# Kernel tuning notes

Hardware: AMD Instinct MI355X
Metric: run time of the kernel (lower is better)

The kernel has to match this reference:

```python
import jax, jax.numpy as jnp
import numpy as np

H, C, PQ, PV = 12, 16, 4, 8
CN = 384
INF, EPS = 1e5, 1e-7


def setup_inputs() -> dict:
    key = jax.random.key(0)
    ks = jax.random.split(key, 12)
    B, N = 2, 768
    s = jax.random.normal(ks[0], (B, N, CN), jnp.float32)
    m = jax.random.normal(ks[1], (B, N, 3, 3), jnp.float32)
    rot, _ = jnp.linalg.qr(m)  # proper orthonormal frames
    trans = jax.random.normal(ks[2], (B, N, 3), jnp.float32)
    pair_mask = jnp.ones((B, N, N), jnp.float32)
    sc = 0.02
    hc = H * C
    w_q = jax.random.normal(ks[3], (hc, CN), jnp.float32) * sc
    b_q = jnp.zeros((hc,), jnp.float32)
    w_kv = jax.random.normal(ks[4], (2 * hc, CN), jnp.float32) * sc
    b_kv = jnp.zeros((2 * hc,), jnp.float32)
    w_qp = jax.random.normal(ks[5], (H * PQ * 3, CN), jnp.float32) * sc
    b_qp = jnp.zeros((H * PQ * 3,), jnp.float32)
    w_kvp = jax.random.normal(ks[6], (H * (PQ + PV) * 3, CN), jnp.float32) * sc
    b_kvp = jnp.zeros((H * (PQ + PV) * 3,), jnp.float32)
    head_weights = jnp.full((H,), float(np.log(np.e - 1.0)), jnp.float32)  # softplus -> 1
    cod = H * (C + PV * 4)
    w_out = jax.random.normal(ks[7], (CN, cod), jnp.float32) * sc
    b_out = jnp.zeros((CN,), jnp.float32)
    return dict(s=s, rot=rot, trans=trans, pair_mask=pair_mask,
                w_q=w_q, b_q=b_q, w_kv=w_kv, b_kv=b_kv,
                w_qp=w_qp, b_qp=b_qp, w_kvp=w_kvp, b_kvp=b_kvp,
                head_weights=head_weights, w_out=w_out, b_out=b_out)


def reference(s, rot, trans, pair_mask, w_q, b_q, w_kv, b_kv, w_qp, b_qp,
              w_kvp, b_kvp, head_weights, w_out, b_out):
    B, N, _ = s.shape
    q = (s @ w_q.T + b_q).reshape(B, N, H, C)
    kv = (s @ w_kv.T + b_kv).reshape(B, N, H, 2 * C)
    k, v = kv[..., :C], kv[..., C:]

    def point_proj(wf, bf, P):
        p = s @ wf.T + bf                                   # [B,N,H*P*3]
        p = jnp.stack(jnp.split(p, 3, axis=-1), axis=-1)     # [B,N,H*P,3]
        p = jnp.einsum('bnxy,bnpy->bnpx', rot, p) + trans[:, :, None, :]
        return p.reshape(B, N, H, P, 3)

    q_pts = point_proj(w_qp, b_qp, PQ)
    kv_pts = point_proj(w_kvp, b_kvp, PQ + PV)
    k_pts, v_pts = kv_pts[..., :PQ, :], kv_pts[..., PQ:, :]

    a = jnp.einsum('bihc,bjhc->bhij', q, k) * (1.0 / (3 * C)) ** 0.5
    # [B,N,N,H,PQ] squared point distances (the big intermediate)
    d2 = jnp.sum((q_pts[:, :, None] - k_pts[:, None]) ** 2, axis=-1)
    hw = jax.nn.softplus(head_weights) * (1.0 / (3 * (PQ * 9.0 / 2))) ** 0.5
    pt_att = -0.5 * jnp.sum(d2 * hw[:, None], axis=-1)      # [B,N,N,H]
    a = a + jnp.transpose(pt_att, (0, 3, 1, 2)) + (INF * (pair_mask - 1.0))[:, None]
    a = jax.nn.softmax(a, axis=-1)                          # [B,H,N,N]

    o = jnp.einsum('bhij,bjhc->bihc', a, v).reshape(B, N, H * C)
    o_pt = jnp.einsum('bhij,bjhpc->bihpc', a, v_pts)        # [B,N,H,PV,3]
    o_pt = jnp.einsum('bnyx,bnhpy->bnhpx', rot, o_pt - trans[:, :, None, None, :])
    o_pt_norm = jnp.sqrt(jnp.sum(o_pt ** 2, axis=-1) + EPS).reshape(B, N, H * PV)
    o_pt = o_pt.reshape(B, N, H * PV, 3)
    cat = jnp.concatenate([o, o_pt[..., 0], o_pt[..., 1], o_pt[..., 2], o_pt_norm], axis=-1)
    return cat @ w_out.T + b_out
```

## Files before the change

kernel.cpp:

```cpp
#include <hip/hip_runtime.h>
#include <hip/hip_bf16.h>
#include <math.h>

typedef __attribute__((ext_vector_type(4)))  short short4v;
typedef __attribute__((ext_vector_type(8)))  short short8;
typedef __attribute__((ext_vector_type(16))) float f32x16;

#define B_   2
#define N_   768
#define CN_  384
#define H_   12
#define INF_ 100000.0f
#define EPS_ 1e-7f

#define OFF_PROJ 0
#define OFF_O    589824
#define OFF_OP   737280
#define OFF_CAT  958464
#define OFF_QF   1769472
#define OFF_KF   2064384
#define OFF_VT   2359296
#define OFF_SB   2949120
#define OFF_WB   3244032
#define OFF_WOB  3465216
#define OFF_MB   3575808

__device__ inline float b2f(unsigned short u) {
    union { unsigned int i; float f; } x; x.i = ((unsigned int)u) << 16; return x.f;
}
__device__ inline unsigned short f2b(float f) {
    __hip_bfloat16 h = __float2bfloat16(f);
    return *reinterpret_cast<unsigned short*>(&h);
}

__global__ __launch_bounds__(256) void prep_kernel(
    const float* __restrict__ s,
    const float* __restrict__ w_q,  const float* __restrict__ w_kv,
    const float* __restrict__ w_qp, const float* __restrict__ w_kvp,
    const float* __restrict__ w_out,
    unsigned short* __restrict__ SB, unsigned short* __restrict__ WB,
    unsigned short* __restrict__ WOBT)
{
    const long i4 = ((long)blockIdx.x * 256 + threadIdx.x) * 4;
    const float* src; unsigned short* dst; long off;
    if (i4 < 589824) {
        src = s + i4; dst = SB; off = i4;
    } else if (i4 < 1032192) {
        long e = i4 - 589824;
        int row = (int)(e / 384), c = (int)(e - (long)row * 384);
        const float* wsrc;
        if (row < 192)      wsrc = w_q   + (long)row * 384;
        else if (row < 576) wsrc = w_kv  + (long)(row - 192) * 384;
        else if (row < 720) wsrc = w_qp  + (long)(row - 576) * 384;
        else                wsrc = w_kvp + (long)(row - 720) * 384;
        src = wsrc + c; dst = WB; off = e;
    } else {
        long e = i4 - 1032192;
        int row = (int)(e / 576), c = (int)(e - (long)row * 576);
        src = w_out + e; dst = WOBT;
        off = (((long)(row >> 5) * 72 + (c >> 3)) * 32 + (row & 31)) * 8 + (c & 7);
    }
    float4 v = *(const float4*)src;
    short4v o;
    o[0] = (short)f2b(v.x); o[1] = (short)f2b(v.y);
    o[2] = (short)f2b(v.z); o[3] = (short)f2b(v.w);
    *(short4v*)(dst + off) = o;
}

__global__ __launch_bounds__(64) void proj_mb_kernel(
    const unsigned short* __restrict__ SB, const unsigned short* __restrict__ WB,
    const float* __restrict__ b_q,  const float* __restrict__ b_kv,
    const float* __restrict__ b_qp, const float* __restrict__ b_kvp,
    const float* __restrict__ mask,
    float* __restrict__ proj, unsigned short* __restrict__ MB)
{
    if (blockIdx.x >= 1728) {
        const int tile = blockIdx.x - 1728;
        const int jt = tile % 24;
        const int it = (tile / 24) % 24;
        const int b  = tile / 576;
        const int tt = threadIdx.x;
        const int i0 = it * 32, j0 = jt * 32;
        const float* mrow = mask + ((long)b * N_ + i0 + (tt & 31)) * N_
                          + j0 + (tt >> 5) * 4;
        union { unsigned short u[16]; short8 v[2]; } o;
        #pragma unroll
        for (int g = 0; g < 4; ++g) {
            float4 mv = *(const float4*)(mrow + 8 * g);
            o.u[g*4+0] = f2b(INF_ * (mv.x - 1.f));
            o.u[g*4+1] = f2b(INF_ * (mv.y - 1.f));
            o.u[g*4+2] = f2b(INF_ * (mv.z - 1.f));
            o.u[g*4+3] = f2b(INF_ * (mv.w - 1.f));
        }
        unsigned short* outp = MB + (long)tile * 1024 + tt * 16;
        *(short8*)(outp)     = o.v[0];
        *(short8*)(outp + 8) = o.v[1];
        return;
    }
    const int tile = blockIdx.x;
    const int tn = tile % 36, tm = tile / 36;
    const int r0 = tm * 32, c0 = tn * 32;
    const int l  = threadIdx.x;
    const int li = l & 31, hf = l >> 5;

    const unsigned short* ap = SB + (long)(r0 + li) * CN_ + hf * 8;
    const int col = c0 + li;
    const unsigned short* wb = WB + (long)col * CN_ + hf * 8;
    const float bias = (col < 192) ? b_q[col] : (col < 576) ? b_kv[col - 192]
                     : (col < 720) ? b_qp[col - 576] : b_kvp[col - 720];

    f32x16 acc = {};
    for (int k = 0; k < CN_; k += 32) {
        short8 a0 = *(const short8*)(ap + k);
        short8 a1 = *(const short8*)(ap + k + 16);
        short8 b0 = *(const short8*)(wb + k);
        short8 b1 = *(const short8*)(wb + k + 16);
        acc = __builtin_amdgcn_mfma_f32_32x32x16_bf16(a0, b0, acc, 0, 0, 0);
        acc = __builtin_amdgcn_mfma_f32_32x32x16_bf16(a1, b1, acc, 0, 0, 0);
    }
    #pragma unroll
    for (int r = 0; r < 16; ++r) {
        int row = r0 + (r & 3) + 8 * (r >> 2) + 4 * hf;
        proj[(long)row * 1152 + col] = acc[r] + bias;
    }
}

__global__ __launch_bounds__(256) void pack2_kernel(
    const float* __restrict__ proj,
    const float* __restrict__ rot, const float* __restrict__ trans,
    const float* __restrict__ head_weights,
    unsigned short* __restrict__ Qf, unsigned short* __restrict__ Kf,
    unsigned short* __restrict__ Vt)
{
    __shared__ float raw[1152];
    __shared__ float pk[1152];
    __shared__ float rt[12];
    __shared__ float hws[12];
    __shared__ float kcs[12];
    const int bn = blockIdx.x;
    const int t  = threadIdx.x;
    const float* rowg = proj + (long)bn * 1152;
    for (int d = t; d < 288; d += 256)
        ((float4*)raw)[d] = ((const float4*)rowg)[d];
    if (t < 9) rt[t]     = rot[bn * 9 + t];
    if (t < 3) rt[9 + t] = trans[bn * 3 + t];
    if (t < 12) {
        float v  = head_weights[t];
        float sp = (v > 20.f) ? v : log1pf(expf(v));
        hws[t] = sp * 0.13608276348795434f;
    }
    __syncthreads();
    for (int slot = t; slot < 1152; slot += 256) {
        int hh = slot / 96, o = slot - hh * 96;
        float val;
        if (o < 16) {
            val = raw[hh * 16 + o] * 0.144337567297406f;
        } else if (o < 28) {
            int c = o - 16, p = c / 3, x = c - p * 3;
            float r0 = raw[576 +      hh * 4 + p];
            float r1 = raw[576 + 48 + hh * 4 + p];
            float r2 = raw[576 + 96 + hh * 4 + p];
            val = (rt[x*3]*r0 + rt[x*3+1]*r1 + rt[x*3+2]*r2 + rt[9+x]) * hws[hh];
        } else if (o < 44) {
            val = raw[192 + hh * 32 + (o - 28)];
        } else if (o < 56) {
            int c = o - 44, p = c / 3, x = c - p * 3;
            float r0 = raw[720 +       hh * 12 + p];
            float r1 = raw[720 + 144 + hh * 12 + p];
            float r2 = raw[720 + 288 + hh * 12 + p];
            val = rt[x*3]*r0 + rt[x*3+1]*r1 + rt[x*3+2]*r2 + rt[9+x];
        } else if (o < 72) {
            val = raw[192 + hh * 32 + 16 + (o - 56)];
        } else {
            int c = o - 72, p = c / 3, x = c - p * 3;
            float r0 = raw[720 +       hh * 12 + 4 + p];
            float r1 = raw[720 + 144 + hh * 12 + 4 + p];
            float r2 = raw[720 + 288 + hh * 12 + 4 + p];
            val = rt[x*3]*r0 + rt[x*3+1]*r1 + rt[x*3+2]*r2 + rt[9+x];
        }
        pk[slot] = val;
    }
    __syncthreads();
    if (t < 12) {
        float s2 = 0.f;
        #pragma unroll
        for (int e = 0; e < 12; ++e) { float v = pk[t * 96 + 44 + e]; s2 += v * v; }
        kcs[t] = -0.5f * hws[t] * s2;
    }
    __syncthreads();
    const int b = bn / N_, n = bn % N_;
    for (int d = t; d < 384; d += 256) {
        int hh = d >> 5, slot = d & 31;
        long base = ((long)(b * H_ + hh) * N_ + n) * 32 + slot;
        float qv, kv;
        if (slot < 28)      qv = pk[hh * 96 + slot];
        else if (slot < 30) qv = 1.f;
        else                qv = 0.f;
        if (slot < 16)      kv = pk[hh * 96 + 28 + slot];
        else if (slot < 28) kv = pk[hh * 96 + 44 + (slot - 16)];
        else if (slot == 28) kv = b2f(f2b(kcs[hh]));
        else if (slot == 29) kv = kcs[hh] - b2f(f2b(kcs[hh]));
        else                kv = 0.f;
        Qf[base] = f2b(qv);
        Kf[base] = f2b(kv);
    }
    for (int d = t; d < 480; d += 256) {
        int hh = d / 40, dd = d - hh * 40;
        Vt[(((long)(b * H_ + hh) * 24 + (n >> 5)) * 64 + dd) * 32 + (n & 31)]
            = f2b(pk[hh * 96 + 56 + dd]);
    }
}

__global__ __launch_bounds__(512) void attn2_kernel(
    const unsigned short* __restrict__ Qf, const unsigned short* __restrict__ Kf,
    const unsigned short* __restrict__ Vt, const unsigned short* __restrict__ MB,
    unsigned short* __restrict__ Og, unsigned short* __restrict__ OPg)
{
    __shared__ float red[8][64][23];
    const int blk = blockIdx.x;
    const int it = blk % 24;
    const int bh = blk / 24;
    const int hh = bh % 12;
    const int b  = bh / 12;
    const int t  = threadIdx.x;
    const int w  = t >> 6;
    const int l  = t & 63;
    const int li = l & 31;
    const int hf = l >> 5;
    const int i0 = it * 32;

    const unsigned short* qbase = Qf + ((long)bh * N_ + i0 + li) * 32 + hf * 8;
    short8 q0 = *(const short8*)(qbase);
    short8 q1 = *(const short8*)(qbase + 16);

    f32x16 acc0 = {};
    f32x16 acc1 = {};
    float m = -1e30f, lsum = 0.f;
    const unsigned short* vtb = Vt + (long)bh * 24 * 2048;
    const unsigned short* mbb = MB + ((long)(b * 24 + it)) * 24 * 1024;

    for (int jt = w * 3; jt < w * 3 + 3; ++jt) {
        const int j0 = jt * 32;
        const unsigned short* mbp = mbb + (long)jt * 1024 + l * 16;
        short8 mb0 = *(const short8*)(mbp);
        short8 mb1 = *(const short8*)(mbp + 8);
        f32x16 S;
        #pragma unroll
        for (int r = 0; r < 8; ++r) S[r]     = b2f((unsigned short)mb0[r]);
        #pragma unroll
        for (int r = 0; r < 8; ++r) S[8 + r] = b2f((unsigned short)mb1[r]);
        const unsigned short* kp = Kf + ((long)bh * N_ + j0 + li) * 32 + hf * 8;
        short8 k0 = *(const short8*)(kp);
        short8 k1 = *(const short8*)(kp + 16);
        S = __builtin_amdgcn_mfma_f32_32x32x16_bf16(k0, q0, S, 0, 0, 0);
        S = __builtin_amdgcn_mfma_f32_32x32x16_bf16(k1, q1, S, 0, 0, 0);
        float mloc = S[0];
        #pragma unroll
        for (int r = 1; r < 16; ++r) mloc = fmaxf(mloc, S[r]);
        {
            auto mm = __builtin_amdgcn_permlane32_swap(
                __float_as_int(mloc), __float_as_int(mloc), false, false);
            mloc = fmaxf(__int_as_float(mm[0]), __int_as_float(mm[1]));
        }
        float newm = fmaxf(m, mloc);
        float scale = __expf(m - newm);
        float ps = 0.f;
        f32x16 p;
        #pragma unroll
        for (int r = 0; r < 16; ++r) { p[r] = __expf(S[r] - newm); ps += p[r]; }
        {
            auto ss = __builtin_amdgcn_permlane32_swap(
                __float_as_int(ps), __float_as_int(ps), false, false);
            ps = __int_as_float(ss[0]) + __int_as_float(ss[1]);
        }
        lsum = lsum * scale + ps;
        m = newm;
        #pragma unroll
        for (int r = 0; r < 16; ++r) acc0[r] *= scale;
        #pragma unroll
        for (int r = 0; r < 4; ++r)  acc1[r] *= scale;
        int c[8];
        #pragma unroll
        for (int r = 0; r < 8; ++r) {
            asm("v_cvt_pk_bf16_f32 %0, %1, %2" : "=v"(c[r]) : "v"(p[2*r]), "v"(p[2*r+1]));
        }
        union { int w4[4]; short8 v; } bf0, bf1;
        bf0.w4[0] = c[0]; bf0.w4[1] = c[1]; bf0.w4[2] = c[2]; bf0.w4[3] = c[3];
        bf1.w4[0] = c[4]; bf1.w4[1] = c[5]; bf1.w4[2] = c[6]; bf1.w4[3] = c[7];
        const unsigned short* tb  = vtb + jt * 2048;
        const unsigned short* vr0 = tb + li * 32 + hf * 4;
        const unsigned short* vr1 = tb + (32 + li) * 32 + hf * 4;
        union { short4v h[2]; short8 v; } v00, v01, v10, v11;
        v00.h[0] = *(const short4v*)(vr0);       v00.h[1] = *(const short4v*)(vr0 + 8);
        v01.h[0] = *(const short4v*)(vr1);       v01.h[1] = *(const short4v*)(vr1 + 8);
        v10.h[0] = *(const short4v*)(vr0 + 16);  v10.h[1] = *(const short4v*)(vr0 + 24);
        v11.h[0] = *(const short4v*)(vr1 + 16);  v11.h[1] = *(const short4v*)(vr1 + 24);
        acc0 = __builtin_amdgcn_mfma_f32_32x32x16_bf16(v00.v, bf0.v, acc0, 0, 0, 0);
        acc1 = __builtin_amdgcn_mfma_f32_32x32x16_bf16(v01.v, bf0.v, acc1, 0, 0, 0);
        acc0 = __builtin_amdgcn_mfma_f32_32x32x16_bf16(v10.v, bf1.v, acc0, 0, 0, 0);
        acc1 = __builtin_amdgcn_mfma_f32_32x32x16_bf16(v11.v, bf1.v, acc1, 0, 0, 0);
    }
    float* rd = &red[w][l][0];
    rd[0] = m; rd[1] = lsum;
    #pragma unroll
    for (int r = 0; r < 16; ++r) rd[2 + r]  = acc0[r];
    #pragma unroll
    for (int r = 0; r < 4; ++r)  rd[18 + r] = acc1[r];
    __syncthreads();
    {
        const int l2 = t & 63, g = t >> 6;
        const int li2 = l2 & 31, hf2 = l2 >> 5;
        float ms = -1e30f;
        #pragma unroll
        for (int ww = 0; ww < 8; ++ww) ms = fmaxf(ms, red[ww][l2][0]);
        float wt[8]; float lf = 0.f;
        #pragma unroll
        for (int ww = 0; ww < 8; ++ww) {
            wt[ww] = __expf(red[ww][l2][0] - ms);
            lf += wt[ww] * red[ww][l2][1];
        }
        float inv = 1.f / lf;
        const int n = i0 + li2;
        #pragma unroll
        for (int rr = 0; rr < 3; ++rr) {
            int r = g + rr * 8;
            if (r < 20) {
                float v = 0.f;
                #pragma unroll
                for (int ww = 0; ww < 8; ++ww) v += wt[ww] * red[ww][l2][2 + r];
                v *= inv;
                int d = (r < 16) ? ((r & 3) + 8 * (r >> 2) + 4 * hf2)
                                 : (32 + (r - 16) + 4 * hf2);
                unsigned short ov = f2b(v);
                if (d < 16) Og [((long)(b * N_ + n)) * 192 + hh * 16 + d] = ov;
                else        OPg[((long)(b * N_ + n)) * 288 + hh * 24 + (d - 16)] = ov;
            }
        }
    }
}

__global__ __launch_bounds__(128) void cat_kernel(
    const unsigned short* __restrict__ Og, const unsigned short* __restrict__ OPg,
    const float* __restrict__ rot, const float* __restrict__ trans,
    unsigned short* __restrict__ catgT)
{
    __shared__ float cat[576];
    __shared__ float rt[12];
    const int bn = blockIdx.x;
    const int t  = threadIdx.x;
    if (t < 9) rt[t]     = rot[bn * 9 + t];
    if (t < 3) rt[9 + t] = trans[bn * 3 + t];
    for (int d = t; d < 192; d += 128) cat[d] = b2f(Og[(long)bn * 192 + d]);
    __syncthreads();
    if (t < 96) {
        float g0 = b2f(OPg[(long)bn * 288 + t * 3 + 0]) - rt[9];
        float g1 = b2f(OPg[(long)bn * 288 + t * 3 + 1]) - rt[10];
        float g2 = b2f(OPg[(long)bn * 288 + t * 3 + 2]) - rt[11];
        float l0 = rt[0]*g0 + rt[3]*g1 + rt[6]*g2;
        float l1 = rt[1]*g0 + rt[4]*g1 + rt[7]*g2;
        float l2 = rt[2]*g0 + rt[5]*g1 + rt[8]*g2;
        cat[192 + t] = l0;
        cat[288 + t] = l1;
        cat[384 + t] = l2;
        cat[480 + t] = sqrtf(l0*l0 + l1*l1 + l2*l2 + EPS_);
    }
    __syncthreads();
    const long sbase = ((long)(bn >> 5)) * 72 * 256 + (bn & 31) * 8;
    for (int d = t; d < 576; d += 128)
        catgT[sbase + (long)(d >> 3) * 256 + (d & 7)] = f2b(cat[d]);
}

__global__ __launch_bounds__(64) void out_mfma(
    const unsigned short* __restrict__ catgT,
    const unsigned short* __restrict__ WOBT,
    const float* __restrict__ b_out,
    float* __restrict__ out)
{
    const int tile = blockIdx.x;
    const int tn = tile % 12, tm = tile / 12;
    const int r0 = tm * 32, c0 = tn * 32;
    const int l  = threadIdx.x;
    const int li = l & 31, hf = l >> 5;

    const unsigned short* ab = catgT + (long)tm * 72 * 256;
    const unsigned short* wb = WOBT  + (long)tn * 72 * 256;

    f32x16 acc = {};
    for (int k = 0; k < 576; k += 32) {
        const int c = (k >> 3) + hf;
        short8 a0 = *(const short8*)(ab + (c * 32 + li) * 8);
        short8 a1 = *(const short8*)(ab + ((c + 2) * 32 + li) * 8);
        short8 b0 = *(const short8*)(wb + (c * 32 + li) * 8);
        short8 b1 = *(const short8*)(wb + ((c + 2) * 32 + li) * 8);
        acc = __builtin_amdgcn_mfma_f32_32x32x16_bf16(a0, b0, acc, 0, 0, 0);
        acc = __builtin_amdgcn_mfma_f32_32x32x16_bf16(a1, b1, acc, 0, 0, 0);
    }
    float bias = b_out[c0 + li];
    #pragma unroll
    for (int r = 0; r < 16; ++r) {
        int row = r0 + (r & 3) + 8 * (r >> 2) + 4 * hf;
        out[(long)row * 384 + c0 + li] = acc[r] + bias;
    }
}

extern "C" void kernel_launch(void* const* d_in, const int* in_sizes, int n_in,
                              void* d_out, int out_size, void* d_ws, size_t ws_size,
                              hipStream_t stream) {
    const float* s            = (const float*)d_in[0];
    const float* rot          = (const float*)d_in[1];
    const float* trans        = (const float*)d_in[2];
    const float* pair_mask    = (const float*)d_in[3];
    const float* w_q          = (const float*)d_in[4];
    const float* b_q          = (const float*)d_in[5];
    const float* w_kv         = (const float*)d_in[6];
    const float* b_kv         = (const float*)d_in[7];
    const float* w_qp         = (const float*)d_in[8];
    const float* b_qp         = (const float*)d_in[9];
    const float* w_kvp        = (const float*)d_in[10];
    const float* b_kvp        = (const float*)d_in[11];
    const float* head_weights = (const float*)d_in[12];
    const float* w_out        = (const float*)d_in[13];
    const float* b_out        = (const float*)d_in[14];
    float* out = (float*)d_out;
    float* ws  = (float*)d_ws;

    float*          PROJ = ws + OFF_PROJ;
    unsigned short* Og   = (unsigned short*)(ws + OFF_O);
    unsigned short* OPg  = (unsigned short*)(ws + OFF_OP);
    unsigned short* CATT = (unsigned short*)(ws + OFF_CAT);
    unsigned short* Qf   = (unsigned short*)(ws + OFF_QF);
    unsigned short* Kf   = (unsigned short*)(ws + OFF_KF);
    unsigned short* Vt   = (unsigned short*)(ws + OFF_VT);
    unsigned short* SB   = (unsigned short*)(ws + OFF_SB);
    unsigned short* WB   = (unsigned short*)(ws + OFF_WB);
    unsigned short* WOBT = (unsigned short*)(ws + OFF_WOB);
    unsigned short* MBp  = (unsigned short*)(ws + OFF_MB);

    prep_kernel<<<1224, 256, 0, stream>>>(s, w_q, w_kv, w_qp, w_kvp, w_out,
                                          SB, WB, WOBT);
    proj_mb_kernel<<<48 * 36 + B_ * 24 * 24, 64, 0, stream>>>(
        SB, WB, b_q, b_kv, b_qp, b_kvp, pair_mask, PROJ, MBp);
    pack2_kernel<<<B_ * N_, 256, 0, stream>>>(PROJ, rot, trans, head_weights,
                                              Qf, Kf, Vt);
    attn2_kernel<<<B_ * H_ * 24, 512, 0, stream>>>(Qf, Kf, Vt, MBp, Og, OPg);
    cat_kernel<<<B_ * N_, 128, 0, stream>>>(Og, OPg, rot, trans, CATT);
    out_mfma<<<48 * 12, 64, 0, stream>>>(CATT, WOBT, b_out, out);
}
```

Before: 61.35 us.

## Write scalar Q/K/V directly from projection GEMM epilogue, shrink pack kernel to points

The projection GEMM epilogue now writes the scalar q (pre-scaled), k and v columns straight into the bf16 Qf/Kf/Vt attention layouts. Only the point-projection columns go to an fp32 staging buffer, so the pack kernel reads 576 floats per row instead of 1152. The pack kernel now handles only the rigid transforms, the key point norm constant and the padding slots, using 128 threads. This cuts fp32 intermediate traffic and pack work, at the cost of scattered bf16 stores in the GEMM epilogue.

```diff
diff --git a/kernel.cpp b/kernel.cpp
--- a/kernel.cpp
+++ b/kernel.cpp
@@ -13,17 +13,17 @@
 #define INF_ 100000.0f
 #define EPS_ 1e-7f
 
-#define OFF_PROJ 0
-#define OFF_O    589824
-#define OFF_OP   737280
-#define OFF_CAT  958464
-#define OFF_QF   1769472
-#define OFF_KF   2064384
-#define OFF_VT   2359296
-#define OFF_SB   2949120
-#define OFF_WB   3244032
-#define OFF_WOB  3465216
-#define OFF_MB   3575808
+#define OFF_PROJP 0
+#define OFF_O     884736
+#define OFF_OP    1032192
+#define OFF_CAT   1253376
+#define OFF_QF    1769472
+#define OFF_KF    2064384
+#define OFF_VT    2359296
+#define OFF_SB    2949120
+#define OFF_WB    3244032
+#define OFF_WOB   3465216
+#define OFF_MB    3575808
 
 __device__ inline float b2f(unsigned short u) {
     union { unsigned int i; float f; } x; x.i = ((unsigned int)u) << 16; return x.f;
@@ -72,7 +72,9 @@
     const float* __restrict__ b_q,  const float* __restrict__ b_kv,
     const float* __restrict__ b_qp, const float* __restrict__ b_kvp,
     const float* __restrict__ mask,
-    float* __restrict__ proj, unsigned short* __restrict__ MB)
+    float* __restrict__ PROJP, unsigned short* __restrict__ Qf,
+    unsigned short* __restrict__ Kf, unsigned short* __restrict__ Vt,
+    unsigned short* __restrict__ MB)
 {
     if (blockIdx.x >= 1728) {
         const int tile = blockIdx.x - 1728;
@@ -118,30 +120,53 @@
         acc = __builtin_amdgcn_mfma_f32_32x32x16_bf16(a0, b0, acc, 0, 0, 0);
         acc = __builtin_amdgcn_mfma_f32_32x32x16_bf16(a1, b1, acc, 0, 0, 0);
     }
-    #pragma unroll
-    for (int r = 0; r < 16; ++r) {
-        int row = r0 + (r & 3) + 8 * (r >> 2) + 4 * hf;
-        proj[(long)row * 1152 + col] = acc[r] + bias;
-    }
-}
-
-__global__ __launch_bounds__(256) void pack2_kernel(
-    const float* __restrict__ proj,
+    const int row_b = r0 / N_;
+    if (tn < 6) {
+        const int hq = col >> 4, c = col & 15;
+        const long qb = (long)(row_b * H_ + hq) * N_;
+        #pragma unroll
+        for (int r = 0; r < 16; ++r) {
+            int row = r0 + (r & 3) + 8 * (r >> 2) + 4 * hf;
+            int n = row - row_b * N_;
+            Qf[(qb + n) * 32 + c] = f2b((acc[r] + bias) * 0.144337567297406f);
+        }
+    } else if (tn < 18) {
+        const int hkv = tn - 6;
+        const long kb = (long)(row_b * H_ + hkv) * N_;
+        const long vb = (long)(row_b * H_ + hkv) * 24;
+        #pragma unroll
+        for (int r = 0; r < 16; ++r) {
+            int row = r0 + (r & 3) + 8 * (r >> 2) + 4 * hf;
+            int n = row - row_b * N_;
+            unsigned short v = f2b(acc[r] + bias);
+            if (li < 16) Kf[(kb + n) * 32 + li] = v;
+            else Vt[((vb + (n >> 5)) * 64 + (li - 16)) * 32 + (n & 31)] = v;
+        }
+    } else {
+        const int pc = col - 576;
+        #pragma unroll
+        for (int r = 0; r < 16; ++r) {
+            int row = r0 + (r & 3) + 8 * (r >> 2) + 4 * hf;
+            PROJP[(long)row * 576 + pc] = acc[r] + bias;
+        }
+    }
+}
+
+__global__ __launch_bounds__(128) void pack3_kernel(
+    const float* __restrict__ PROJP,
     const float* __restrict__ rot, const float* __restrict__ trans,
     const float* __restrict__ head_weights,
     unsigned short* __restrict__ Qf, unsigned short* __restrict__ Kf,
     unsigned short* __restrict__ Vt)
 {
-    __shared__ float raw[1152];
-    __shared__ float pk[1152];
+    __shared__ float pp[576];
     __shared__ float rt[12];
     __shared__ float hws[12];
-    __shared__ float kcs[12];
+    __shared__ float kp2[48];
     const int bn = blockIdx.x;
     const int t  = threadIdx.x;
-    const float* rowg = proj + (long)bn * 1152;
-    for (int d = t; d < 288; d += 256)
-        ((float4*)raw)[d] = ((const float4*)rowg)[d];
+    const float4* src = (const float4*)(PROJP + (long)bn * 576);
+    for (int d = t; d < 144; d += 128) ((float4*)pp)[d] = src[d];
     if (t < 9) rt[t]     = rot[bn * 9 + t];
     if (t < 3) rt[9 + t] = trans[bn * 3 + t];
     if (t < 12) {
@@ -150,64 +175,55 @@
         hws[t] = sp * 0.13608276348795434f;
     }
     __syncthreads();
-    for (int slot = t; slot < 1152; slot += 256) {
-        int hh = slot / 96, o = slot - hh * 96;
-        float val;
-        if (o < 16) {
-            val = raw[hh * 16 + o] * 0.144337567297406f;
-        } else if (o < 28) {
-            int c = o - 16, p = c / 3, x = c - p * 3;
-            float r0 = raw[576 +      hh * 4 + p];
-            float r1 = raw[576 + 48 + hh * 4 + p];
-            float r2 = raw[576 + 96 + hh * 4 + p];
-            val = (rt[x*3]*r0 + rt[x*3+1]*r1 + rt[x*3+2]*r2 + rt[9+x]) * hws[hh];
-        } else if (o < 44) {
-            val = raw[192 + hh * 32 + (o - 28)];
-        } else if (o < 56) {
-            int c = o - 44, p = c / 3, x = c - p * 3;
-            float r0 = raw[720 +       hh * 12 + p];
-            float r1 = raw[720 + 144 + hh * 12 + p];
-            float r2 = raw[720 + 288 + hh * 12 + p];
-            val = rt[x*3]*r0 + rt[x*3+1]*r1 + rt[x*3+2]*r2 + rt[9+x];
-        } else if (o < 72) {
-            val = raw[192 + hh * 32 + 16 + (o - 56)];
+    const int b = bn / N_, n = bn % N_;
+    for (int e = t; e < 192; e += 128) {
+        if (e < 48) {
+            int h = e >> 2, p = e & 3;
+            float r0 = pp[     h * 4 + p];
+            float r1 = pp[48 + h * 4 + p];
+            float r2 = pp[96 + h * 4 + p];
+            long base = ((long)(b * H_ + h) * N_ + n) * 32;
+            #pragma unroll
+            for (int x = 0; x < 3; ++x) {
+                float o = rt[x*3]*r0 + rt[x*3+1]*r1 + rt[x*3+2]*r2 + rt[9+x];
+                Qf[base + 16 + p * 3 + x] = f2b(o * hws[h]);
+            }
         } else {
-            int c = o - 72, p = c / 3, x = c - p * 3;
-            float r0 = raw[720 +       hh * 12 + 4 + p];
-            float r1 = raw[720 + 144 + hh * 12 + 4 + p];
-            float r2 = raw[720 + 288 + hh * 12 + 4 + p];
-            val = rt[x*3]*r0 + rt[x*3+1]*r1 + rt[x*3+2]*r2 + rt[9+x];
-        }
-        pk[slot] = val;
+            int idx = e - 48;
+            int h = idx / 12, pi = idx - h * 12;
+            float r0 = pp[144 +       h * 12 + pi];
+            float r1 = pp[144 + 144 + h * 12 + pi];
+            float r2 = pp[144 + 288 + h * 12 + pi];
+            float o0 = rt[0]*r0 + rt[1]*r1 + rt[2]*r2 + rt[9];
+            float o1 = rt[3]*r0 + rt[4]*r1 + rt[5]*r2 + rt[10];
+            float o2 = rt[6]*r0 + rt[7]*r1 + rt[8]*r2 + rt[11];
+            if (pi < 4) {
+                long base = ((long)(b * H_ + h) * N_ + n) * 32;
+                Kf[base + 16 + pi * 3 + 0] = f2b(o0);
+                Kf[base + 16 + pi * 3 + 1] = f2b(o1);
+                Kf[base + 16 + pi * 3 + 2] = f2b(o2);
+                kp2[h * 4 + pi] = o0*o0 + o1*o1 + o2*o2;
+            } else {
+                int dd = 16 + (pi - 4) * 3;
+                long vb = ((long)(b * H_ + h) * 24 + (n >> 5)) * 64;
+                Vt[(vb + dd + 0) * 32 + (n & 31)] = f2b(o0);
+                Vt[(vb + dd + 1) * 32 + (n & 31)] = f2b(o1);
+                Vt[(vb + dd + 2) * 32 + (n & 31)] = f2b(o2);
+            }
+        }
     }
     __syncthreads();
     if (t < 12) {
-        float s2 = 0.f;
-        #pragma unroll
-        for (int e = 0; e < 12; ++e) { float v = pk[t * 96 + 44 + e]; s2 += v * v; }
-        kcs[t] = -0.5f * hws[t] * s2;
-    }
-    __syncthreads();
-    const int b = bn / N_, n = bn % N_;
-    for (int d = t; d < 384; d += 256) {
-        int hh = d >> 5, slot = d & 31;
-        long base = ((long)(b * H_ + hh) * N_ + n) * 32 + slot;
-        float qv, kv;
-        if (slot < 28)      qv = pk[hh * 96 + slot];
-        else if (slot < 30) qv = 1.f;
-        else                qv = 0.f;
-        if (slot < 16)      kv = pk[hh * 96 + 28 + slot];
-        else if (slot < 28) kv = pk[hh * 96 + 44 + (slot - 16)];
-        else if (slot == 28) kv = b2f(f2b(kcs[hh]));
-        else if (slot == 29) kv = kcs[hh] - b2f(f2b(kcs[hh]));
-        else                kv = 0.f;
-        Qf[base] = f2b(qv);
-        Kf[base] = f2b(kv);
-    }
-    for (int d = t; d < 480; d += 256) {
-        int hh = d / 40, dd = d - hh * 40;
-        Vt[(((long)(b * H_ + hh) * 24 + (n >> 5)) * 64 + dd) * 32 + (n & 31)]
-            = f2b(pk[hh * 96 + 56 + dd]);
+        float s2 = kp2[t*4] + kp2[t*4+1] + kp2[t*4+2] + kp2[t*4+3];
+        float kc = -0.5f * hws[t] * s2;
+        long base = ((long)(b * H_ + t) * N_ + n) * 32;
+        unsigned short hi = f2b(kc);
+        Kf[base + 28] = hi;
+        Kf[base + 29] = f2b(kc - b2f(hi));
+        Kf[base + 30] = 0; Kf[base + 31] = 0;
+        unsigned short one = f2b(1.f);
+        Qf[base + 28] = one; Qf[base + 29] = one;
+        Qf[base + 30] = 0;   Qf[base + 31] = 0;
     }
 }
 
@@ -424,7 +440,7 @@
     float* out = (float*)d_out;
     float* ws  = (float*)d_ws;
 
-    float*          PROJ = ws + OFF_PROJ;
+    float*          PROJP = ws + OFF_PROJP;
     unsigned short* Og   = (unsigned short*)(ws + OFF_O);
     unsigned short* OPg  = (unsigned short*)(ws + OFF_OP);
     unsigned short* CATT = (unsigned short*)(ws + OFF_CAT);
@@ -439,8 +455,8 @@
     prep_kernel<<<1224, 256, 0, stream>>>(s, w_q, w_kv, w_qp, w_kvp, w_out,
                                           SB, WB, WOBT);
     proj_mb_kernel<<<48 * 36 + B_ * 24 * 24, 64, 0, stream>>>(
-        SB, WB, b_q, b_kv, b_qp, b_kvp, pair_mask, PROJ, MBp);
-    pack2_kernel<<<B_ * N_, 256, 0, stream>>>(PROJ, rot, trans, head_weights,
+        SB, WB, b_q, b_kv, b_qp, b_kvp, pair_mask, PROJP, Qf, Kf, Vt, MBp);
+    pack3_kernel<<<B_ * N_, 128, 0, stream>>>(PROJP, rot, trans, head_weights,
                                               Qf, Kf, Vt);
     attn2_kernel<<<B_ * H_ * 24, 512, 0, stream>>>(Qf, Kf, Vt, MBp, Og, OPg);
     cat_kernel<<<B_ * N_, 128, 0, stream>>>(Og, OPg, rot, trans, CATT);
```

After: 57.69 us. -6.0%, faster.
